# Performance work log

Measured on AMD Instinct MI355X. Metric: run time of the kernel, lower is better.

Reference implementation:

```python
import jax, jax.numpy as jnp
import numpy as np

B, N, NS, D, H = 32, 4096, 16, 512, 8
DH = D // H          # dims_per_head = 64
DFF = 4 * D          # ff_mlp hidden
SCALE = DH ** -0.5
EPS = 1e-8           # slot-attention renorm eps
LN_EPS = 1e-5        # torch LayerNorm default
ITERS = 3


def layer_norm(x, g, b):
    mu = jnp.mean(x, axis=-1, keepdims=True)
    var = jnp.mean((x - mu) ** 2, axis=-1, keepdims=True)
    return (x - mu) * jax.lax.rsqrt(var + LN_EPS) * g + b


def setup_inputs() -> dict:
    key = jax.random.key(0)
    ks = jax.random.split(key, 8)
    s = 0.02
    return {
        "inputs": jax.random.normal(ks[0], (B, N, D), jnp.float32),
        "conditioning": jax.random.normal(ks[1], (B, NS, D), jnp.float32),
        # norm_input
        "ln_in_g": jnp.ones((D,), jnp.float32),
        "ln_in_b": jnp.zeros((D,), jnp.float32),
        # projections (no bias: use_projection_bias=False)
        "Wk": jax.random.normal(ks[2], (D, D), jnp.float32) * s,
        "Wv": jax.random.normal(ks[3], (D, D), jnp.float32) * s,
        "Wq": jax.random.normal(ks[4], (D, D), jnp.float32) * s,
        "Wo": jax.random.normal(ks[5], (D, D), jnp.float32) * s,
        # norm_slots / norm_slots_ff_mlp
        "ln_s_g": jnp.ones((D,), jnp.float32),
        "ln_s_b": jnp.zeros((D,), jnp.float32),
        "ln_f_g": jnp.ones((D,), jnp.float32),
        "ln_f_b": jnp.zeros((D,), jnp.float32),
        # ff_mlp: Linear(D,4D) -> ReLU -> Linear(4D,D)
        "W1": jax.random.normal(ks[6], (D, DFF), jnp.float32) * s,
        "b1": jnp.zeros((DFF,), jnp.float32),
        "W2": jax.random.normal(ks[7], (DFF, D), jnp.float32) * s,
        "b2": jnp.zeros((D,), jnp.float32),
    }


def reference(inputs, conditioning, ln_in_g, ln_in_b, Wk, Wv, Wq, Wo,
              ln_s_g, ln_s_b, ln_f_g, ln_f_b, W1, b1, W2, b2):
    b = inputs.shape[0]
    x = layer_norm(inputs, ln_in_g, ln_in_b)                 # [b, n, D]
    k = (x @ Wk.T).reshape(b, N, H, DH)                      # [b, n, h, dh]
    v = (x @ Wv.T).reshape(b, N, H, DH)

    slots = conditioning
    attn_mean = None
    for _ in range(ITERS):
        slots_prev = slots
        s = layer_norm(slots, ln_s_g, ln_s_b)
        q = (s @ Wq.T).reshape(b, NS, H, DH)                 # [b, ns, h, dh]
        dots = jnp.einsum("bihd,bjhd->bihj", q, k) * SCALE   # [b, ns, h, n]
        # softmax over flattened (slots, heads) axis, per input location j
        attn = jax.nn.softmax(dots.reshape(b, NS * H, N), axis=1)
        attn = attn.reshape(b, NS, H, N)
        attn_before = attn
        attn = attn + EPS
        attn = attn / jnp.sum(attn, axis=-1, keepdims=True)  # renorm over j
        updates = jnp.einsum("bjhd,bihj->bihd", v, attn)     # [b, ns, h, dh]
        updates = updates.reshape(b, NS, D)
        slots = updates @ Wo.T + slots_prev                  # to_o + residual
        slots_prev_ff = slots
        s2 = layer_norm(slots, ln_f_g, ln_f_b)
        s2 = jax.nn.relu(s2 @ W1 + b1) @ W2 + b2             # ff_mlp
        slots = s2 + slots_prev_ff
        attn_mean = jnp.mean(attn_before, axis=2)            # [b, ns, n]
    return slots, attn_mean
```

## Files before the change

### kernel.cpp

```cpp
#include <hip/hip_runtime.h>
#include <cstdint>
#include <cstddef>

typedef __attribute__((ext_vector_type(8))) short short8;
typedef __attribute__((ext_vector_type(4))) short short4v;
typedef __attribute__((ext_vector_type(8))) __bf16 bf16x8;
typedef __attribute__((ext_vector_type(4))) float f32x4;
typedef unsigned short u16;

static constexpr int Bb = 32, Nn = 4096, NSs = 16, Dd = 512, Hh = 8, DFF = 2048;
static constexpr float SCALE = 0.125f;
static constexpr float EPSR  = 1e-8f;
static constexpr float LN_EPS = 1e-5f;

__device__ __forceinline__ u16 f2b(float x) {
  union { float f; uint32_t u; } a; a.f = x;
  uint32_t r = a.u + 0x7fffu + ((a.u >> 16) & 1u);
  return (u16)(r >> 16);
}

__device__ __forceinline__ f32x4 mfma16(short8 a, short8 b, f32x4 c) {
  return __builtin_amdgcn_mfma_f32_16x16x32_bf16(
      __builtin_bit_cast(bf16x8, a), __builtin_bit_cast(bf16x8, b), c, 0, 0, 0);
}

__device__ __forceinline__ void gload16(const u16* g, u16* l) {
  __builtin_amdgcn_global_load_lds(
      (const __attribute__((address_space(1))) void*)g,
      (__attribute__((address_space(3))) void*)l, 16, 0, 0);
}

__global__ __launch_bounds__(256) void ln_rows(const float* __restrict__ src,
    const float* __restrict__ g, const float* __restrict__ bt,
    u16* __restrict__ dst, int R) {
  int row = blockIdx.x * 4 + (threadIdx.x >> 6);
  if (row >= R) return;
  int lane = threadIdx.x & 63;
  const float* p = src + (size_t)row * Dd + lane * 8;
  float4 u0 = *(const float4*)p;
  float4 u1 = *(const float4*)(p + 4);
  float x[8] = {u0.x,u0.y,u0.z,u0.w,u1.x,u1.y,u1.z,u1.w};
  float s = 0.f, s2 = 0.f;
#pragma unroll
  for (int e = 0; e < 8; ++e) { s += x[e]; s2 += x[e]*x[e]; }
#pragma unroll
  for (int m = 1; m < 64; m <<= 1) { s += __shfl_xor(s, m); s2 += __shfl_xor(s2, m); }
  float mean = s * (1.f/512.f);
  float var  = s2 * (1.f/512.f) - mean*mean;
  float rstd = rsqrtf(var + LN_EPS);
  union { u16 o[8]; short8 v; } ou;
#pragma unroll
  for (int e = 0; e < 8; ++e)
    ou.o[e] = f2b((x[e]-mean)*rstd*g[lane*8+e] + bt[lane*8+e]);
  *(short8*)(dst + (size_t)row * Dd + lane * 8) = ou.v;
}

__global__ __launch_bounds__(256, 2) void gemm_kv(const u16* __restrict__ A,
    const u16* __restrict__ Bk, const u16* __restrict__ Bv,
    u16* __restrict__ Ck, u16* __restrict__ CvT) {
  __shared__ u16 lA[128*64];
  __shared__ u16 lK[128*64];
  __shared__ u16 lV[128*64];
  const int tid = threadIdx.x, lane = tid & 63, wid = tid >> 6;
  const int wr = wid >> 1, wc = wid & 1;
  const int n  = blockIdx.y * 4 + blockIdx.x;
  const int orig = (n & 7) * 512 + (n >> 3);
  const int bm = (orig >> 2) * 128, bn = (orig & 3) * 128;
  const size_t BN = (size_t)Bb * Nn;
  f32x4 ak[4][4] = {};
  f32x4 av[4][4] = {};
  const int sr = lane >> 3;
  const int ss = ((lane & 7) ^ (sr & 7)) * 8;
  const int li = lane & 15, lk = lane >> 4;
  const int sx = (li & 7) * 8;
  for (int t = 0; t < 8; ++t) {
    const int k0 = t * 64;
    __syncthreads();
#pragma unroll
    for (int gi = 0; gi < 4; ++gi) {
      const int rb = wid * 32 + gi * 8;
      gload16(A  + (size_t)(bm + rb + sr) * Dd + k0 + ss, &lA[rb * 64]);
      gload16(Bk + (size_t)(bn + rb + sr) * Dd + k0 + ss, &lK[rb * 64]);
      gload16(Bv + (size_t)(bn + rb + sr) * Dd + k0 + ss, &lV[rb * 64]);
    }
    __syncthreads();
#pragma unroll
    for (int kk = 0; kk < 2; ++kk) {
      const int cs = ((kk * 4 + lk) * 8) ^ sx;
      short8 af[4], kf[4], vf[4];
#pragma unroll
      for (int m = 0; m < 4; ++m)
        af[m] = *(const short8*)&lA[(wr*64 + m*16 + li)*64 + cs];
#pragma unroll
      for (int nn2 = 0; nn2 < 4; ++nn2) {
        kf[nn2] = *(const short8*)&lK[(wc*64 + nn2*16 + li)*64 + cs];
        vf[nn2] = *(const short8*)&lV[(wc*64 + nn2*16 + li)*64 + cs];
      }
#pragma unroll
      for (int m = 0; m < 4; ++m)
#pragma unroll
        for (int nn2 = 0; nn2 < 4; ++nn2) {
          ak[m][nn2] = mfma16(af[m], kf[nn2], ak[m][nn2]);
          av[m][nn2] = mfma16(af[m], vf[nn2], av[m][nn2]);
        }
    }
  }
  const int lr = lk * 4;
#pragma unroll
  for (int m = 0; m < 4; ++m)
#pragma unroll
    for (int nn2 = 0; nn2 < 4; ++nn2) {
      int row = bm + wr*64 + m*16 + lr;
      int col = bn + wc*64 + nn2*16 + li;
      f32x4 vk = ak[m][nn2];
#pragma unroll
      for (int r = 0; r < 4; ++r)
        Ck[(size_t)(row + r) * Dd + col] = f2b(vk[r]);
      f32x4 vv = av[m][nn2];
      union { u16 o[4]; short4v v4; } ou;
#pragma unroll
      for (int r = 0; r < 4; ++r) ou.o[r] = f2b(vv[r]);
      *(short4v*)&CvT[(size_t)col * BN + row] = ou.v4;
    }
}

template<int EP>
__global__ __launch_bounds__(256) void gemm64(const u16* __restrict__ A,
    const u16* __restrict__ Bw, void* __restrict__ Cp,
    const float* __restrict__ bias, const float* __restrict__ res,
    int N, int K) {
  __shared__ u16 lA[2][64*32];
  __shared__ u16 lB[2][64*32];
  const int tid = threadIdx.x, lane = tid & 63, wid = tid >> 6;
  const int wr = wid >> 1, wc = wid & 1;
  const int bm = blockIdx.y * 64, bn = blockIdx.x * 64;
  f32x4 acc[2][2] = {};
  const int srow = wid*16 + (lane >> 2);
  const int scol = ((lane & 3) ^ ((lane >> 3) & 3)) * 8;
  const u16* Ap = A + (size_t)(bm + srow) * K + scol;
  const u16* Bp = Bw + (size_t)(bn + srow) * K + scol;
  const int ldb = wid * 512;
  const int li = lane & 15, lk = lane >> 4;
  const int csw = (lk ^ ((li >> 1) & 3)) * 8;
  const int nsteps = K >> 5;
  gload16(Ap, &lA[0][ldb]);
  gload16(Bp, &lB[0][ldb]);
  int cur = 0;
  for (int t = 0; t < nsteps; ++t) {
    __syncthreads();
    const int nx = cur ^ 1;
    if (t + 1 < nsteps) {
      const int k0 = (t + 1) * 32;
      gload16(Ap + k0, &lA[nx][ldb]);
      gload16(Bp + k0, &lB[nx][ldb]);
    }
    short8 af[2], bf[2];
#pragma unroll
    for (int m = 0; m < 2; ++m)
      af[m] = *(const short8*)&lA[cur][(wr*32 + m*16 + li)*32 + csw];
#pragma unroll
    for (int nn2 = 0; nn2 < 2; ++nn2)
      bf[nn2] = *(const short8*)&lB[cur][(wc*32 + nn2*16 + li)*32 + csw];
#pragma unroll
    for (int m = 0; m < 2; ++m)
#pragma unroll
      for (int nn2 = 0; nn2 < 2; ++nn2)
        acc[m][nn2] = mfma16(af[m], bf[nn2], acc[m][nn2]);
    cur = nx;
  }
  const int lr = lk * 4;
#pragma unroll
  for (int m = 0; m < 2; ++m)
#pragma unroll
    for (int nn2 = 0; nn2 < 2; ++nn2) {
      int row = bm + wr*32 + m*16 + lr;
      int col = bn + wc*32 + nn2*16 + li;
      f32x4 v = acc[m][nn2];
#pragma unroll
      for (int r = 0; r < 4; ++r) {
        size_t off = (size_t)(row + r) * N + col;
        float x = v[r];
        if constexpr (EP == 0) ((u16*)Cp)[off] = f2b(x);
        else if constexpr (EP == 1) ((float*)Cp)[off] = x + res[off];
        else if constexpr (EP == 2) { x += bias[col]; ((u16*)Cp)[off] = f2b(x > 0.f ? x : 0.f); }
        else ((float*)Cp)[off] = x + bias[col] + res[off];
      }
    }
}

__global__ __launch_bounds__(256) void attn_a(const u16* __restrict__ q,
    const u16* __restrict__ kk, u16* __restrict__ attnb,
    float* __restrict__ rowsum, float* __restrict__ attn_mean) {
  const int jt = blockIdx.x, b = blockIdx.y;
  const int tid = threadIdx.x, lane = tid & 63, wid = tid >> 6;
  __shared__ float sc[64][129];
  __shared__ float red[4][64];
  const int li = lane & 15, lk = lane >> 4;
#pragma unroll
  for (int hh = 0; hh < 2; ++hh) {
    const int h = wid * 2 + hh;
    const u16* qb = q + (((size_t)b*16 + li)*8 + h)*64 + lk*8;
    short8 a0 = *(const short8*)qb;
    short8 a1 = *(const short8*)(qb + 32);
#pragma unroll
    for (int n = 0; n < 4; ++n) {
      const u16* kb = kk + ((size_t)b*Nn + jt*64 + n*16 + li)*Dd + h*64 + lk*8;
      f32x4 acc = {};
      acc = mfma16(a0, *(const short8*)kb, acc);
      acc = mfma16(a1, *(const short8*)(kb + 32), acc);
#pragma unroll
      for (int r = 0; r < 4; ++r)
        sc[n*16 + li][(lk*4 + r)*8 + h] = acc[r] * SCALE;
    }
  }
  __syncthreads();
  const int jl = tid & 63, qt = tid >> 6;
  float mx = -1e30f;
#pragma unroll
  for (int e = 0; e < 32; ++e) mx = fmaxf(mx, sc[jl][qt*32 + e]);
  red[qt][jl] = mx;
  __syncthreads();
  float M = fmaxf(fmaxf(red[0][jl], red[1][jl]), fmaxf(red[2][jl], red[3][jl]));
  __syncthreads();
  float s = 0.f;
#pragma unroll
  for (int e = 0; e < 32; ++e) {
    float ev = __expf(sc[jl][qt*32 + e] - M);
    sc[jl][qt*32 + e] = ev; s += ev;
  }
  red[qt][jl] = s;
  __syncthreads();
  float S = red[0][jl] + red[1][jl] + red[2][jl] + red[3][jl];
  float inv = 1.f / S;
#pragma unroll
  for (int e = 0; e < 32; ++e)
    sc[jl][qt*32 + e] = sc[jl][qt*32 + e] * inv + EPSR;
  __syncthreads();
  if (tid < 128) {
    float rs = 0.f;
    for (int j2 = 0; j2 < 64; ++j2) rs += sc[j2][tid];
    atomicAdd(&rowsum[b*128 + tid], rs);
  }
#pragma unroll
  for (int e = 0; e < 32; ++e) {
    int r = qt*32 + e;
    attnb[((size_t)b*128 + r)*Nn + jt*64 + jl] = f2b(sc[jl][r]);
  }
  if (attn_mean != nullptr && tid < 64) {
    for (int i = 0; i < 16; ++i) {
      float sm = 0.f;
#pragma unroll
      for (int h = 0; h < 8; ++h) sm += sc[tid][i*8 + h];
      attn_mean[((size_t)b*16 + i)*Nn + jt*64 + tid] = sm * 0.125f - EPSR;
    }
  }
}

__global__ __launch_bounds__(256) void attn_b(const u16* __restrict__ attnb,
    const u16* __restrict__ vT, float* __restrict__ Tpart) {
  const int h = blockIdx.x, js = blockIdx.y, b = blockIdx.z;
  const int lane = threadIdx.x & 63, wid = threadIdx.x >> 6;
  const int li = lane & 15, lk = lane >> 4;
  const size_t BN = (size_t)Bb * Nn;
  const int j0 = js * 1024;
  const u16* Ap = attnb + ((size_t)b*128 + li*8 + h)*Nn + j0 + lk*8;
  const u16* Bp = vT + (size_t)(h*64 + wid*16 + li)*BN + (size_t)b*Nn + j0 + lk*8;
  f32x4 acc[4] = {};
  for (int k0 = 0; k0 < 1024; k0 += 128) {
#pragma unroll
    for (int e = 0; e < 4; ++e)
      acc[e] = mfma16(*(const short8*)(Ap + k0 + e*32),
                      *(const short8*)(Bp + k0 + e*32), acc[e]);
  }
  float* Tout = Tpart + ((((size_t)js * Bb + b) * 8 + h) * 16) * 64;
#pragma unroll
  for (int r = 0; r < 4; ++r) {
    int i = lk*4 + r;
    float t = acc[0][r] + acc[1][r] + acc[2][r] + acc[3][r];
    Tout[(size_t)i * 64 + wid*16 + li] = t;
  }
}

__global__ void upd_c(const float* __restrict__ Tpart,
    const float* __restrict__ rs, u16* __restrict__ updb) {
  int idx = blockIdx.x * 256 + threadIdx.x;
  int o = idx & 511, bi = idx >> 9;
  int b = bi >> 4, i = bi & 15;
  int h = o >> 6, d = o & 63;
  size_t base = (((size_t)b * 8 + h) * 16 + i) * 64 + d;
  const size_t stride = (size_t)Bb * 8 * 16 * 64;
  float t = Tpart[base] + Tpart[base + stride]
          + Tpart[base + 2*stride] + Tpart[base + 3*stride];
  updb[idx] = f2b(t / rs[b * 128 + i * 8 + h]);
}

__global__ void cvt_w(const float* __restrict__ s, u16* __restrict__ d, int n) {
  int i = blockIdx.x*256 + threadIdx.x;
  if (i < n) d[i] = f2b(s[i]);
}
__global__ __launch_bounds__(256) void tr_cvt(const float* __restrict__ s,
    u16* __restrict__ d, int R, int C) {
  __shared__ u16 t[32][33];
  const int c0 = blockIdx.x*32, r0 = blockIdx.y*32;
  const int tr = threadIdx.x >> 3, tc4 = (threadIdx.x & 7)*4;
  float4 v = *(const float4*)&s[(size_t)(r0+tr)*C + c0 + tc4];
  t[tr][tc4+0] = f2b(v.x); t[tr][tc4+1] = f2b(v.y);
  t[tr][tc4+2] = f2b(v.z); t[tr][tc4+3] = f2b(v.w);
  __syncthreads();
  const int oc = threadIdx.x >> 3, or4 = (threadIdx.x & 7)*4;
  union { u16 o[4]; short4v v4; } ou;
#pragma unroll
  for (int e = 0; e < 4; ++e) ou.o[e] = t[or4+e][oc];
  *(short4v*)&d[(size_t)(c0+oc)*R + r0 + or4] = ou.v4;
}
__global__ void copy_f32v4(const float* __restrict__ s, float* __restrict__ d, int n4) {
  int i = blockIdx.x*256 + threadIdx.x;
  if (i < n4) ((float4*)d)[i] = ((const float4*)s)[i];
}

extern "C" void kernel_launch(void* const* d_in, const int* in_sizes, int n_in,
                              void* d_out, int out_size, void* d_ws, size_t ws_size,
                              hipStream_t stream) {
  (void)in_sizes; (void)n_in; (void)out_size; (void)ws_size;
  const float* inputs  = (const float*)d_in[0];
  const float* cond    = (const float*)d_in[1];
  const float* ln_in_g = (const float*)d_in[2];
  const float* ln_in_b = (const float*)d_in[3];
  const float* Wk = (const float*)d_in[4];
  const float* Wv = (const float*)d_in[5];
  const float* Wq = (const float*)d_in[6];
  const float* Wo = (const float*)d_in[7];
  const float* ln_s_g = (const float*)d_in[8];
  const float* ln_s_b = (const float*)d_in[9];
  const float* ln_f_g = (const float*)d_in[10];
  const float* ln_f_b = (const float*)d_in[11];
  const float* W1 = (const float*)d_in[12];
  const float* b1 = (const float*)d_in[13];
  const float* W2 = (const float*)d_in[14];
  const float* b2 = (const float*)d_in[15];
  float* out_slots = (float*)d_out;
  float* out_amean = (float*)d_out + (size_t)Bb*NSs*Dd;

  char* w = (char*)d_ws;
  auto alloc = [&](size_t bytes) {
    char* p = w; w += (bytes + 255) & ~(size_t)255; return p;
  };
  u16*  xn    = (u16*)alloc((size_t)Bb*Nn*Dd*2);
  u16*  kbuf  = (u16*)alloc((size_t)Bb*Nn*Dd*2);
  u16*  vT    = (u16*)alloc((size_t)Bb*Nn*Dd*2);
  u16*  attnb = (u16*)alloc((size_t)Bb*128*Nn*2);
  float* Tpart = (float*)alloc((size_t)4*Bb*8*16*64*4);
  float* slots = (float*)alloc((size_t)Bb*NSs*Dd*4);
  u16*  qb    = (u16*)alloc((size_t)Bb*NSs*Dd*2);
  u16*  snb   = (u16*)alloc((size_t)Bb*NSs*Dd*2);
  u16*  s2nb  = (u16*)alloc((size_t)Bb*NSs*Dd*2);
  u16*  h1b   = (u16*)alloc((size_t)Bb*NSs*DFF*2);
  u16*  updb  = (u16*)alloc((size_t)Bb*NSs*Dd*2);
  float* rowsum = (float*)alloc((size_t)Bb*128*3*4);
  u16*  wkb = (u16*)alloc(262144*2);
  u16*  wvb = (u16*)alloc(262144*2);
  u16*  wqb = (u16*)alloc(262144*2);
  u16*  wob = (u16*)alloc(262144*2);
  u16*  w1t = (u16*)alloc((size_t)1048576*2);
  u16*  w2t = (u16*)alloc((size_t)1048576*2);

  cvt_w<<<1024, 256, 0, stream>>>(Wk, wkb, 262144);
  cvt_w<<<1024, 256, 0, stream>>>(Wv, wvb, 262144);
  cvt_w<<<1024, 256, 0, stream>>>(Wq, wqb, 262144);
  cvt_w<<<1024, 256, 0, stream>>>(Wo, wob, 262144);
  tr_cvt<<<dim3(64, 16), 256, 0, stream>>>(W1, w1t, 512, 2048);
  tr_cvt<<<dim3(16, 64), 256, 0, stream>>>(W2, w2t, 2048, 512);
  copy_f32v4<<<256, 256, 0, stream>>>(cond, slots, 65536);
  (void)hipMemsetAsync(rowsum, 0, (size_t)Bb*128*3*4, stream);
  ln_rows<<<Bb*Nn/4, 256, 0, stream>>>(inputs, ln_in_g, ln_in_b, xn, Bb*Nn);
  gemm_kv<<<dim3(4, Bb*Nn/128), 256, 0, stream>>>(xn, wkb, wvb, kbuf, vT);

  for (int it = 0; it < 3; ++it) {
    float* rsp = rowsum + (size_t)it * Bb * 128;
    ln_rows<<<128, 256, 0, stream>>>(slots, ln_s_g, ln_s_b, snb, Bb*NSs);
    gemm64<0><<<dim3(8, 8), 256, 0, stream>>>(snb, wqb, qb, nullptr, nullptr, 512, 512);
    attn_a<<<dim3(Nn/64, Bb), 256, 0, stream>>>(qb, kbuf, attnb, rsp,
                                                it == 2 ? out_amean : nullptr);
    attn_b<<<dim3(Hh, 4, Bb), 256, 0, stream>>>(attnb, vT, Tpart);
    upd_c<<<1024, 256, 0, stream>>>(Tpart, rsp, updb);
    gemm64<1><<<dim3(8, 8), 256, 0, stream>>>(updb, wob, slots, nullptr, slots, 512, 512);
    ln_rows<<<128, 256, 0, stream>>>(slots, ln_f_g, ln_f_b, s2nb, Bb*NSs);
    gemm64<2><<<dim3(32, 8), 256, 0, stream>>>(s2nb, w1t, h1b, b1, nullptr, 2048, 512);
    gemm64<3><<<dim3(8, 8), 256, 0, stream>>>(h1b, w2t, slots, b2, slots, 512, 2048);
  }
  copy_f32v4<<<256, 256, 0, stream>>>(slots, out_slots, 65536);
}
```

Baseline: 706.3 us.

## Double-buffer KV projection GEMM with explicit vmcnt waits and barriers

The K/V projection GEMM goes from single-buffered 64-wide K tiles with two __syncthreads per step to double-buffered 32-wide K tiles. The next tile's global-to-LDS loads are issued before computing the current one, using explicit s_waitcnt vmcnt and raw s_barrier with sched_barrier fences, and MFMA priority is raised via s_setprio. The small generic GEMM gets the same explicit-waitcnt and barrier treatment. The goal is to overlap global loads with MFMA work. In exchange there are twice as many loop iterations, hand-counted vmcnt values that depend on each gload16 being exactly one vmem op, and a second barrier per step.

```diff
diff --git a/kernel.cpp b/kernel.cpp
--- a/kernel.cpp
+++ b/kernel.cpp
@@ -58,9 +58,9 @@
 __global__ __launch_bounds__(256, 2) void gemm_kv(const u16* __restrict__ A,
     const u16* __restrict__ Bk, const u16* __restrict__ Bv,
     u16* __restrict__ Ck, u16* __restrict__ CvT) {
-  __shared__ u16 lA[128*64];
-  __shared__ u16 lK[128*64];
-  __shared__ u16 lV[128*64];
+  __shared__ u16 lA[2][128*32];
+  __shared__ u16 lK[2][128*32];
+  __shared__ u16 lV[2][128*32];
   const int tid = threadIdx.x, lane = tid & 63, wid = tid >> 6;
   const int wr = wid >> 1, wc = wid & 1;
   const int n  = blockIdx.y * 4 + blockIdx.x;
@@ -69,42 +69,58 @@
   const size_t BN = (size_t)Bb * Nn;
   f32x4 ak[4][4] = {};
   f32x4 av[4][4] = {};
-  const int sr = lane >> 3;
-  const int ss = ((lane & 7) ^ (sr & 7)) * 8;
+  const int srow = wid*16 + (lane >> 2);
+  const int scol = ((lane & 3) ^ ((lane >> 3) & 3)) * 8;
+  const u16* Ap = A  + (size_t)(bm + srow) * Dd + scol;
+  const u16* Kp = Bk + (size_t)(bn + srow) * Dd + scol;
+  const u16* Vp = Bv + (size_t)(bn + srow) * Dd + scol;
+  const int ldb = wid * 512;
   const int li = lane & 15, lk = lane >> 4;
-  const int sx = (li & 7) * 8;
-  for (int t = 0; t < 8; ++t) {
-    const int k0 = t * 64;
-    __syncthreads();
-#pragma unroll
-    for (int gi = 0; gi < 4; ++gi) {
-      const int rb = wid * 32 + gi * 8;
-      gload16(A  + (size_t)(bm + rb + sr) * Dd + k0 + ss, &lA[rb * 64]);
-      gload16(Bk + (size_t)(bn + rb + sr) * Dd + k0 + ss, &lK[rb * 64]);
-      gload16(Bv + (size_t)(bn + rb + sr) * Dd + k0 + ss, &lV[rb * 64]);
-    }
-    __syncthreads();
-#pragma unroll
-    for (int kk = 0; kk < 2; ++kk) {
-      const int cs = ((kk * 4 + lk) * 8) ^ sx;
-      short8 af[4], kf[4], vf[4];
-#pragma unroll
-      for (int m = 0; m < 4; ++m)
-        af[m] = *(const short8*)&lA[(wr*64 + m*16 + li)*64 + cs];
+  const int csw = (lk ^ ((li >> 1) & 3)) * 8;
+#define KV_STAGE(buf, k0) do { \
+    gload16(Ap + (k0), &lA[buf][ldb]); \
+    gload16(Ap + (size_t)64*Dd + (k0), &lA[buf][ldb + 2048]); \
+    gload16(Kp + (k0), &lK[buf][ldb]); \
+    gload16(Kp + (size_t)64*Dd + (k0), &lK[buf][ldb + 2048]); \
+    gload16(Vp + (k0), &lV[buf][ldb]); \
+    gload16(Vp + (size_t)64*Dd + (k0), &lV[buf][ldb + 2048]); \
+  } while (0)
+  KV_STAGE(0, 0);
+  int cur = 0;
+  for (int t = 0; t < 16; ++t) {
+    if (t < 15) {
+      KV_STAGE(cur ^ 1, (t + 1) * 32);
+      asm volatile("s_waitcnt vmcnt(6)" ::: "memory");
+    } else {
+      asm volatile("s_waitcnt vmcnt(0)" ::: "memory");
+    }
+    __builtin_amdgcn_sched_barrier(0);
+    __builtin_amdgcn_s_barrier();
+    __builtin_amdgcn_sched_barrier(0);
+    short8 af[4], kf[4], vf[4];
+#pragma unroll
+    for (int m = 0; m < 4; ++m)
+      af[m] = *(const short8*)&lA[cur][(wr*64 + m*16 + li)*32 + csw];
+#pragma unroll
+    for (int nn2 = 0; nn2 < 4; ++nn2) {
+      kf[nn2] = *(const short8*)&lK[cur][(wc*64 + nn2*16 + li)*32 + csw];
+      vf[nn2] = *(const short8*)&lV[cur][(wc*64 + nn2*16 + li)*32 + csw];
+    }
+    __builtin_amdgcn_s_setprio(1);
+#pragma unroll
+    for (int m = 0; m < 4; ++m)
 #pragma unroll
       for (int nn2 = 0; nn2 < 4; ++nn2) {
-        kf[nn2] = *(const short8*)&lK[(wc*64 + nn2*16 + li)*64 + cs];
-        vf[nn2] = *(const short8*)&lV[(wc*64 + nn2*16 + li)*64 + cs];
+        ak[m][nn2] = mfma16(af[m], kf[nn2], ak[m][nn2]);
+        av[m][nn2] = mfma16(af[m], vf[nn2], av[m][nn2]);
       }
-#pragma unroll
-      for (int m = 0; m < 4; ++m)
-#pragma unroll
-        for (int nn2 = 0; nn2 < 4; ++nn2) {
-          ak[m][nn2] = mfma16(af[m], kf[nn2], ak[m][nn2]);
-          av[m][nn2] = mfma16(af[m], vf[nn2], av[m][nn2]);
-        }
-    }
-  }
+    __builtin_amdgcn_s_setprio(0);
+    __builtin_amdgcn_sched_barrier(0);
+    __builtin_amdgcn_s_barrier();
+    __builtin_amdgcn_sched_barrier(0);
+    cur ^= 1;
+  }
+#undef KV_STAGE
   const int lr = lk * 4;
 #pragma unroll
   for (int m = 0; m < 4; ++m)
@@ -147,13 +163,17 @@
   gload16(Bp, &lB[0][ldb]);
   int cur = 0;
   for (int t = 0; t < nsteps; ++t) {
-    __syncthreads();
-    const int nx = cur ^ 1;
     if (t + 1 < nsteps) {
       const int k0 = (t + 1) * 32;
-      gload16(Ap + k0, &lA[nx][ldb]);
-      gload16(Bp + k0, &lB[nx][ldb]);
-    }
+      gload16(Ap + k0, &lA[cur ^ 1][ldb]);
+      gload16(Bp + k0, &lB[cur ^ 1][ldb]);
+      asm volatile("s_waitcnt vmcnt(2)" ::: "memory");
+    } else {
+      asm volatile("s_waitcnt vmcnt(0)" ::: "memory");
+    }
+    __builtin_amdgcn_sched_barrier(0);
+    __builtin_amdgcn_s_barrier();
+    __builtin_amdgcn_sched_barrier(0);
     short8 af[2], bf[2];
 #pragma unroll
     for (int m = 0; m < 2; ++m)
@@ -161,12 +181,17 @@
 #pragma unroll
     for (int nn2 = 0; nn2 < 2; ++nn2)
       bf[nn2] = *(const short8*)&lB[cur][(wc*32 + nn2*16 + li)*32 + csw];
+    __builtin_amdgcn_s_setprio(1);
 #pragma unroll
     for (int m = 0; m < 2; ++m)
 #pragma unroll
       for (int nn2 = 0; nn2 < 2; ++nn2)
         acc[m][nn2] = mfma16(af[m], bf[nn2], acc[m][nn2]);
-    cur = nx;
+    __builtin_amdgcn_s_setprio(0);
+    __builtin_amdgcn_sched_barrier(0);
+    __builtin_amdgcn_s_barrier();
+    __builtin_amdgcn_sched_barrier(0);
+    cur ^= 1;
   }
   const int lr = lk * 4;
 #pragma unroll
```

New measurement: 705.9 us. Within noise of the previous version (-0.1%).

## Load GEMM weight fragments directly from global memory instead of LDS staging

Applied to the files above, without the earlier changes.

In the K/V projection GEMM, the Wk/Wv tiles are no longer staged through shared memory. Each wave reads its MFMA B-fragments straight from global memory, which relies on the small weight matrices staying cache-resident, and the MFMA block is raised in priority with s_setprio. The small gemm64 kernel drops LDS and double buffering entirely and loads both operands directly from global memory inside an unrolled K loop. This cuts LDS traffic and barriers and raises occupancy, but risks uncoalesced, cache-dependent global loads and exposes load latency to the MFMA loop. The launch grid is also flattened to 1D with the same block remapping.

```diff
diff --git a/kernel.cpp b/kernel.cpp
--- a/kernel.cpp
+++ b/kernel.cpp
@@ -59,43 +59,42 @@
     const u16* __restrict__ Bk, const u16* __restrict__ Bv,
     u16* __restrict__ Ck, u16* __restrict__ CvT) {
   __shared__ u16 lA[128*64];
-  __shared__ u16 lK[128*64];
-  __shared__ u16 lV[128*64];
   const int tid = threadIdx.x, lane = tid & 63, wid = tid >> 6;
   const int wr = wid >> 1, wc = wid & 1;
-  const int n  = blockIdx.y * 4 + blockIdx.x;
+  const int n  = blockIdx.x;
   const int orig = (n & 7) * 512 + (n >> 3);
   const int bm = (orig >> 2) * 128, bn = (orig & 3) * 128;
   const size_t BN = (size_t)Bb * Nn;
   f32x4 ak[4][4] = {};
   f32x4 av[4][4] = {};
-  const int sr = lane >> 3;
-  const int ss = ((lane & 7) ^ (sr & 7)) * 8;
   const int li = lane & 15, lk = lane >> 4;
-  const int sx = (li & 7) * 8;
+  const int sr0 = tid >> 3, ss0 = tid & 7;
+  const u16* Kp = Bk + (size_t)(bn + wc*64 + li) * Dd + lk*8;
+  const u16* Vp = Bv + (size_t)(bn + wc*64 + li) * Dd + lk*8;
   for (int t = 0; t < 8; ++t) {
     const int k0 = t * 64;
     __syncthreads();
 #pragma unroll
-    for (int gi = 0; gi < 4; ++gi) {
-      const int rb = wid * 32 + gi * 8;
-      gload16(A  + (size_t)(bm + rb + sr) * Dd + k0 + ss, &lA[rb * 64]);
-      gload16(Bk + (size_t)(bn + rb + sr) * Dd + k0 + ss, &lK[rb * 64]);
-      gload16(Bv + (size_t)(bn + rb + sr) * Dd + k0 + ss, &lV[rb * 64]);
+    for (int p = 0; p < 4; ++p) {
+      const int rr = p*32 + sr0;
+      gload16(A + (size_t)(bm + rr) * Dd + k0 + ((ss0 ^ (rr & 7)) * 8),
+              &lA[(p*32 + wid*8) * 64]);
     }
     __syncthreads();
 #pragma unroll
-    for (int kk = 0; kk < 2; ++kk) {
-      const int cs = ((kk * 4 + lk) * 8) ^ sx;
+    for (int ks = 0; ks < 2; ++ks) {
+      const int kc = k0 + ks*32;
       short8 af[4], kf[4], vf[4];
 #pragma unroll
       for (int m = 0; m < 4; ++m)
-        af[m] = *(const short8*)&lA[(wr*64 + m*16 + li)*64 + cs];
+        af[m] = *(const short8*)&lA[(wr*64 + m*16 + li)*64
+                                    + (((ks*4 + lk) ^ (li & 7)) * 8)];
 #pragma unroll
       for (int nn2 = 0; nn2 < 4; ++nn2) {
-        kf[nn2] = *(const short8*)&lK[(wc*64 + nn2*16 + li)*64 + cs];
-        vf[nn2] = *(const short8*)&lV[(wc*64 + nn2*16 + li)*64 + cs];
+        kf[nn2] = *(const short8*)(Kp + (size_t)(nn2*16) * Dd + kc);
+        vf[nn2] = *(const short8*)(Vp + (size_t)(nn2*16) * Dd + kc);
       }
+      __builtin_amdgcn_s_setprio(1);
 #pragma unroll
       for (int m = 0; m < 4; ++m)
 #pragma unroll
@@ -103,6 +102,7 @@
           ak[m][nn2] = mfma16(af[m], kf[nn2], ak[m][nn2]);
           av[m][nn2] = mfma16(af[m], vf[nn2], av[m][nn2]);
         }
+      __builtin_amdgcn_s_setprio(0);
     }
   }
   const int lr = lk * 4;
@@ -129,44 +129,25 @@
     const u16* __restrict__ Bw, void* __restrict__ Cp,
     const float* __restrict__ bias, const float* __restrict__ res,
     int N, int K) {
-  __shared__ u16 lA[2][64*32];
-  __shared__ u16 lB[2][64*32];
-  const int tid = threadIdx.x, lane = tid & 63, wid = tid >> 6;
+  const int lane = threadIdx.x & 63, wid = threadIdx.x >> 6;
   const int wr = wid >> 1, wc = wid & 1;
   const int bm = blockIdx.y * 64, bn = blockIdx.x * 64;
+  const int li = lane & 15, lk = lane >> 4;
   f32x4 acc[2][2] = {};
-  const int srow = wid*16 + (lane >> 2);
-  const int scol = ((lane & 3) ^ ((lane >> 3) & 3)) * 8;
-  const u16* Ap = A + (size_t)(bm + srow) * K + scol;
-  const u16* Bp = Bw + (size_t)(bn + srow) * K + scol;
-  const int ldb = wid * 512;
-  const int li = lane & 15, lk = lane >> 4;
-  const int csw = (lk ^ ((li >> 1) & 3)) * 8;
-  const int nsteps = K >> 5;
-  gload16(Ap, &lA[0][ldb]);
-  gload16(Bp, &lB[0][ldb]);
-  int cur = 0;
-  for (int t = 0; t < nsteps; ++t) {
-    __syncthreads();
-    const int nx = cur ^ 1;
-    if (t + 1 < nsteps) {
-      const int k0 = (t + 1) * 32;
-      gload16(Ap + k0, &lA[nx][ldb]);
-      gload16(Bp + k0, &lB[nx][ldb]);
-    }
+  const u16* Ap = A  + (size_t)(bm + wr*32 + li) * K + lk*8;
+  const u16* Bp = Bw + (size_t)(bn + wc*32 + li) * K + lk*8;
+#pragma unroll 4
+  for (int k0 = 0; k0 < K; k0 += 32) {
     short8 af[2], bf[2];
-#pragma unroll
-    for (int m = 0; m < 2; ++m)
-      af[m] = *(const short8*)&lA[cur][(wr*32 + m*16 + li)*32 + csw];
-#pragma unroll
-    for (int nn2 = 0; nn2 < 2; ++nn2)
-      bf[nn2] = *(const short8*)&lB[cur][(wc*32 + nn2*16 + li)*32 + csw];
+    af[0] = *(const short8*)(Ap + k0);
+    af[1] = *(const short8*)(Ap + (size_t)16*K + k0);
+    bf[0] = *(const short8*)(Bp + k0);
+    bf[1] = *(const short8*)(Bp + (size_t)16*K + k0);
 #pragma unroll
     for (int m = 0; m < 2; ++m)
 #pragma unroll
       for (int nn2 = 0; nn2 < 2; ++nn2)
         acc[m][nn2] = mfma16(af[m], bf[nn2], acc[m][nn2]);
-    cur = nx;
   }
   const int lr = lk * 4;
 #pragma unroll
@@ -373,7 +354,7 @@
   copy_f32v4<<<256, 256, 0, stream>>>(cond, slots, 65536);
   (void)hipMemsetAsync(rowsum, 0, (size_t)Bb*128*3*4, stream);
   ln_rows<<<Bb*Nn/4, 256, 0, stream>>>(inputs, ln_in_g, ln_in_b, xn, Bb*Nn);
-  gemm_kv<<<dim3(4, Bb*Nn/128), 256, 0, stream>>>(xn, wkb, wvb, kbuf, vT);
+  gemm_kv<<<4096, 256, 0, stream>>>(xn, wkb, wvb, kbuf, vT);
 
   for (int it = 0; it < 3; ++it) {
     float* rsp = rowsum + (size_t)it * Bb * 128;
```

Measured after the change: 824.4 us. +16.7%, slower.

## Fuse slot softmax and attn·V into one kernel; drop LDS staging in small GEMMs

Applied to the files above, without the earlier changes.

Merges the score/softmax kernel and the attention-times-V kernel into a single kernel per (batch, 512-column chunk). Each wave owns one head and keeps the bf16 attention tile in shared memory, so the attention matrix no longer round-trips through global memory. Row sums are accumulated in registers and written with one atomic per block. The split over the sequence grows from 4 to 8 partials, so the reduction kernel sums 8 slices. Separately, the small 64x64 GEMM now loads operands straight from global memory instead of double-buffered LDS. The fused kernel launches only 256 blocks of 512 threads and serialises 8 tiles with many barriers, which risks lower occupancy and parallelism.

```diff
diff --git a/kernel.cpp b/kernel.cpp
--- a/kernel.cpp
+++ b/kernel.cpp
@@ -129,44 +129,25 @@
     const u16* __restrict__ Bw, void* __restrict__ Cp,
     const float* __restrict__ bias, const float* __restrict__ res,
     int N, int K) {
-  __shared__ u16 lA[2][64*32];
-  __shared__ u16 lB[2][64*32];
-  const int tid = threadIdx.x, lane = tid & 63, wid = tid >> 6;
+  const int lane = threadIdx.x & 63, wid = threadIdx.x >> 6;
   const int wr = wid >> 1, wc = wid & 1;
   const int bm = blockIdx.y * 64, bn = blockIdx.x * 64;
+  const int li = lane & 15, lk = lane >> 4;
   f32x4 acc[2][2] = {};
-  const int srow = wid*16 + (lane >> 2);
-  const int scol = ((lane & 3) ^ ((lane >> 3) & 3)) * 8;
-  const u16* Ap = A + (size_t)(bm + srow) * K + scol;
-  const u16* Bp = Bw + (size_t)(bn + srow) * K + scol;
-  const int ldb = wid * 512;
-  const int li = lane & 15, lk = lane >> 4;
-  const int csw = (lk ^ ((li >> 1) & 3)) * 8;
-  const int nsteps = K >> 5;
-  gload16(Ap, &lA[0][ldb]);
-  gload16(Bp, &lB[0][ldb]);
-  int cur = 0;
-  for (int t = 0; t < nsteps; ++t) {
-    __syncthreads();
-    const int nx = cur ^ 1;
-    if (t + 1 < nsteps) {
-      const int k0 = (t + 1) * 32;
-      gload16(Ap + k0, &lA[nx][ldb]);
-      gload16(Bp + k0, &lB[nx][ldb]);
-    }
+  const u16* Ap = A  + (size_t)(bm + wr*32 + li) * K + lk*8;
+  const u16* Bp = Bw + (size_t)(bn + wc*32 + li) * K + lk*8;
+#pragma unroll 4
+  for (int k0 = 0; k0 < K; k0 += 32) {
     short8 af[2], bf[2];
-#pragma unroll
-    for (int m = 0; m < 2; ++m)
-      af[m] = *(const short8*)&lA[cur][(wr*32 + m*16 + li)*32 + csw];
-#pragma unroll
-    for (int nn2 = 0; nn2 < 2; ++nn2)
-      bf[nn2] = *(const short8*)&lB[cur][(wc*32 + nn2*16 + li)*32 + csw];
+    af[0] = *(const short8*)(Ap + k0);
+    af[1] = *(const short8*)(Ap + (size_t)16*K + k0);
+    bf[0] = *(const short8*)(Bp + k0);
+    bf[1] = *(const short8*)(Bp + (size_t)16*K + k0);
 #pragma unroll
     for (int m = 0; m < 2; ++m)
 #pragma unroll
       for (int nn2 = 0; nn2 < 2; ++nn2)
         acc[m][nn2] = mfma16(af[m], bf[nn2], acc[m][nn2]);
-    cur = nx;
   }
   const int lr = lk * 4;
 #pragma unroll
@@ -188,23 +169,29 @@
     }
 }
 
-__global__ __launch_bounds__(256) void attn_a(const u16* __restrict__ q,
-    const u16* __restrict__ kk, u16* __restrict__ attnb,
-    float* __restrict__ rowsum, float* __restrict__ attn_mean) {
-  const int jt = blockIdx.x, b = blockIdx.y;
-  const int tid = threadIdx.x, lane = tid & 63, wid = tid >> 6;
+__global__ __launch_bounds__(512) void attn_f(const u16* __restrict__ q,
+    const u16* __restrict__ kk, const u16* __restrict__ vT,
+    float* __restrict__ rowsum, float* __restrict__ Tpart,
+    float* __restrict__ attn_mean) {
+  const int js = blockIdx.x, b = blockIdx.y;
+  const int tid = threadIdx.x, lane = tid & 63;
+  const int h = tid >> 6;
   __shared__ float sc[64][129];
-  __shared__ float red[4][64];
+  __shared__ float red[8][64];
+  __shared__ u16 P2[8][16][72];
   const int li = lane & 15, lk = lane >> 4;
-#pragma unroll
-  for (int hh = 0; hh < 2; ++hh) {
-    const int h = wid * 2 + hh;
-    const u16* qb = q + (((size_t)b*16 + li)*8 + h)*64 + lk*8;
-    short8 a0 = *(const short8*)qb;
-    short8 a1 = *(const short8*)(qb + 32);
+  const size_t BN = (size_t)Bb * Nn;
+  const u16* qb = q + (((size_t)b*16 + li)*8 + h)*64 + lk*8;
+  short8 a0 = *(const short8*)qb;
+  short8 a1 = *(const short8*)(qb + 32);
+  f32x4 apv[4] = {};
+  float rs_acc = 0.f;
+  const int jl = tid & 63, qt = tid >> 6;
+  for (int t2 = 0; t2 < 8; ++t2) {
+    const int j0 = js * 512 + t2 * 64;
 #pragma unroll
     for (int n = 0; n < 4; ++n) {
-      const u16* kb = kk + ((size_t)b*Nn + jt*64 + n*16 + li)*Dd + h*64 + lk*8;
+      const u16* kb = kk + ((size_t)b*Nn + j0 + n*16 + li)*Dd + h*64 + lk*8;
       f32x4 acc = {};
       acc = mfma16(a0, *(const short8*)kb, acc);
       acc = mfma16(a1, *(const short8*)(kb + 32), acc);
@@ -212,73 +199,68 @@
       for (int r = 0; r < 4; ++r)
         sc[n*16 + li][(lk*4 + r)*8 + h] = acc[r] * SCALE;
     }
+    __syncthreads();
+    float mx = -1e30f;
+#pragma unroll
+    for (int e = 0; e < 16; ++e) mx = fmaxf(mx, sc[jl][qt*16 + e]);
+    red[qt][jl] = mx;
+    __syncthreads();
+    float M = red[0][jl];
+#pragma unroll
+    for (int p = 1; p < 8; ++p) M = fmaxf(M, red[p][jl]);
+    __syncthreads();
+    float s = 0.f;
+#pragma unroll
+    for (int e = 0; e < 16; ++e) {
+      float ev = __expf(sc[jl][qt*16 + e] - M);
+      sc[jl][qt*16 + e] = ev; s += ev;
+    }
+    red[qt][jl] = s;
+    __syncthreads();
+    float S = red[0][jl];
+#pragma unroll
+    for (int p = 1; p < 8; ++p) S += red[p][jl];
+    float inv = 1.f / S;
+#pragma unroll
+    for (int e = 0; e < 16; ++e) {
+      int ih = qt*16 + e;
+      float a = sc[jl][ih] * inv + EPSR;
+      sc[jl][ih] = a;
+      P2[ih & 7][ih >> 3][jl] = f2b(a);
+    }
+    __syncthreads();
+    if (tid < 128) {
+      float rs = 0.f;
+      for (int j2 = 0; j2 < 64; ++j2) rs += sc[j2][tid];
+      rs_acc += rs;
+    }
+    if (attn_mean != nullptr && tid < 64) {
+      for (int i = 0; i < 16; ++i) {
+        float sm = 0.f;
+#pragma unroll
+        for (int hh = 0; hh < 8; ++hh) sm += sc[tid][i*8 + hh];
+        attn_mean[((size_t)b*16 + i)*Nn + j0 + tid] = sm * 0.125f - EPSR;
+      }
+    }
+#pragma unroll
+    for (int n = 0; n < 4; ++n) {
+      const u16* vb = vT + (size_t)(h*64 + n*16 + li)*BN + (size_t)b*Nn + j0 + lk*8;
+      short8 b0 = *(const short8*)vb;
+      short8 b1 = *(const short8*)(vb + 32);
+      short8 pa0 = *(const short8*)&P2[h][li][lk*8];
+      short8 pa1 = *(const short8*)&P2[h][li][32 + lk*8];
+      apv[n] = mfma16(pa0, b0, apv[n]);
+      apv[n] = mfma16(pa1, b1, apv[n]);
+    }
+    __syncthreads();
   }
-  __syncthreads();
-  const int jl = tid & 63, qt = tid >> 6;
-  float mx = -1e30f;
-#pragma unroll
-  for (int e = 0; e < 32; ++e) mx = fmaxf(mx, sc[jl][qt*32 + e]);
-  red[qt][jl] = mx;
-  __syncthreads();
-  float M = fmaxf(fmaxf(red[0][jl], red[1][jl]), fmaxf(red[2][jl], red[3][jl]));
-  __syncthreads();
-  float s = 0.f;
-#pragma unroll
-  for (int e = 0; e < 32; ++e) {
-    float ev = __expf(sc[jl][qt*32 + e] - M);
-    sc[jl][qt*32 + e] = ev; s += ev;
-  }
-  red[qt][jl] = s;
-  __syncthreads();
-  float S = red[0][jl] + red[1][jl] + red[2][jl] + red[3][jl];
-  float inv = 1.f / S;
-#pragma unroll
-  for (int e = 0; e < 32; ++e)
-    sc[jl][qt*32 + e] = sc[jl][qt*32 + e] * inv + EPSR;
-  __syncthreads();
-  if (tid < 128) {
-    float rs = 0.f;
-    for (int j2 = 0; j2 < 64; ++j2) rs += sc[j2][tid];
-    atomicAdd(&rowsum[b*128 + tid], rs);
-  }
-#pragma unroll
-  for (int e = 0; e < 32; ++e) {
-    int r = qt*32 + e;
-    attnb[((size_t)b*128 + r)*Nn + jt*64 + jl] = f2b(sc[jl][r]);
-  }
-  if (attn_mean != nullptr && tid < 64) {
-    for (int i = 0; i < 16; ++i) {
-      float sm = 0.f;
-#pragma unroll
-      for (int h = 0; h < 8; ++h) sm += sc[tid][i*8 + h];
-      attn_mean[((size_t)b*16 + i)*Nn + jt*64 + tid] = sm * 0.125f - EPSR;
-    }
-  }
-}
-
-__global__ __launch_bounds__(256) void attn_b(const u16* __restrict__ attnb,
-    const u16* __restrict__ vT, float* __restrict__ Tpart) {
-  const int h = blockIdx.x, js = blockIdx.y, b = blockIdx.z;
-  const int lane = threadIdx.x & 63, wid = threadIdx.x >> 6;
-  const int li = lane & 15, lk = lane >> 4;
-  const size_t BN = (size_t)Bb * Nn;
-  const int j0 = js * 1024;
-  const u16* Ap = attnb + ((size_t)b*128 + li*8 + h)*Nn + j0 + lk*8;
-  const u16* Bp = vT + (size_t)(h*64 + wid*16 + li)*BN + (size_t)b*Nn + j0 + lk*8;
-  f32x4 acc[4] = {};
-  for (int k0 = 0; k0 < 1024; k0 += 128) {
-#pragma unroll
-    for (int e = 0; e < 4; ++e)
-      acc[e] = mfma16(*(const short8*)(Ap + k0 + e*32),
-                      *(const short8*)(Bp + k0 + e*32), acc[e]);
-  }
-  float* Tout = Tpart + ((((size_t)js * Bb + b) * 8 + h) * 16) * 64;
-#pragma unroll
-  for (int r = 0; r < 4; ++r) {
-    int i = lk*4 + r;
-    float t = acc[0][r] + acc[1][r] + acc[2][r] + acc[3][r];
-    Tout[(size_t)i * 64 + wid*16 + li] = t;
-  }
+  float* Tout = Tpart + (((size_t)js * Bb + b) * 8 + h) * 16 * 64;
+#pragma unroll
+  for (int n = 0; n < 4; ++n)
+#pragma unroll
+    for (int r = 0; r < 4; ++r)
+      Tout[(size_t)(lk*4 + r) * 64 + n*16 + li] = apv[n][r];
+  if (tid < 128) atomicAdd(&rowsum[b*128 + tid], rs_acc);
 }
 
 __global__ void upd_c(const float* __restrict__ Tpart,
@@ -289,8 +271,9 @@
   int h = o >> 6, d = o & 63;
   size_t base = (((size_t)b * 8 + h) * 16 + i) * 64 + d;
   const size_t stride = (size_t)Bb * 8 * 16 * 64;
-  float t = Tpart[base] + Tpart[base + stride]
-          + Tpart[base + 2*stride] + Tpart[base + 3*stride];
+  float t = 0.f;
+#pragma unroll
+  for (int p = 0; p < 8; ++p) t += Tpart[base + p * stride];
   updb[idx] = f2b(t / rs[b * 128 + i * 8 + h]);
 }
 
@@ -348,8 +331,7 @@
   u16*  xn    = (u16*)alloc((size_t)Bb*Nn*Dd*2);
   u16*  kbuf  = (u16*)alloc((size_t)Bb*Nn*Dd*2);
   u16*  vT    = (u16*)alloc((size_t)Bb*Nn*Dd*2);
-  u16*  attnb = (u16*)alloc((size_t)Bb*128*Nn*2);
-  float* Tpart = (float*)alloc((size_t)4*Bb*8*16*64*4);
+  float* Tpart = (float*)alloc((size_t)8*Bb*8*16*64*4);
   float* slots = (float*)alloc((size_t)Bb*NSs*Dd*4);
   u16*  qb    = (u16*)alloc((size_t)Bb*NSs*Dd*2);
   u16*  snb   = (u16*)alloc((size_t)Bb*NSs*Dd*2);
@@ -379,9 +361,8 @@
     float* rsp = rowsum + (size_t)it * Bb * 128;
     ln_rows<<<128, 256, 0, stream>>>(slots, ln_s_g, ln_s_b, snb, Bb*NSs);
     gemm64<0><<<dim3(8, 8), 256, 0, stream>>>(snb, wqb, qb, nullptr, nullptr, 512, 512);
-    attn_a<<<dim3(Nn/64, Bb), 256, 0, stream>>>(qb, kbuf, attnb, rsp,
-                                                it == 2 ? out_amean : nullptr);
-    attn_b<<<dim3(Hh, 4, Bb), 256, 0, stream>>>(attnb, vT, Tpart);
+    attn_f<<<dim3(8, Bb), 512, 0, stream>>>(qb, kbuf, vT, rsp, Tpart,
+                                            it == 2 ? out_amean : nullptr);
     upd_c<<<1024, 256, 0, stream>>>(Tpart, rsp, updb);
     gemm64<1><<<dim3(8, 8), 256, 0, stream>>>(updb, wob, slots, nullptr, slots, 512, 512);
     ln_rows<<<128, 256, 0, stream>>>(slots, ln_f_g, ln_f_b, s2nb, Bb*NSs);
```

New measurement: 730.2 us. +3.4%, slower.
